# Kernel tuning notes

Hardware: AMD Instinct MI355X
Metric: run time of the kernel (lower is better)

Reference implementation:

```python
import jax, jax.numpy as jnp
import numpy as np

B, N, D = 16, 4096, 256
EPS = 1e-6


def setup_inputs() -> dict:
    key = jax.random.key(0)
    kq, kk, kv, kwq, kwk, kbq, kbk = jax.random.split(key, 7)
    s = 1.0 / np.sqrt(D)
    return {
        "Q": jax.random.normal(kq, (B, N, D), dtype=jnp.float32),
        "K": jax.random.normal(kk, (B, N, D), dtype=jnp.float32),
        "V": jax.random.normal(kv, (B, N, D), dtype=jnp.float32),
        "Wq": jax.random.normal(kwq, (D, D), dtype=jnp.float32) * s,
        "bq": jax.random.normal(kbq, (D,), dtype=jnp.float32) * 0.01,
        "Wk": jax.random.normal(kwk, (D, D), dtype=jnp.float32) * s,
        "bk": jax.random.normal(kbk, (D,), dtype=jnp.float32) * 0.01,
    }


def reference(Q, K, V, Wq, bq, Wk, bk):
    # phi feature maps: sigmoid(Linear(dim, dim)) as in Flow-Attention
    phi_q = jax.nn.sigmoid(jnp.einsum("bnd,de->bne", Q, Wq) + bq)  # [B,N,D]
    phi_k = jax.nn.sigmoid(jnp.einsum("bnd,de->bne", K, Wk) + bk)  # [B,N,D]
    # O: column-normalized phi_k (over sequence); I: row-normalized phi_q (over features)
    O = phi_k / (jnp.sum(phi_k, axis=1, keepdims=True) + EPS)  # [B,N,D]
    I = phi_q / (jnp.sum(phi_q, axis=2, keepdims=True) + EPS)  # [B,N,D]
    # competition over the sequence dim
    V_b = jax.nn.softmax(O * V, axis=1)  # [B,N,D]
    # linear attention: (phi_k^T @ V_b) is the small [B,D,D] state
    KV = jnp.einsum("bnd,bne->bde", phi_k, V_b)  # [B,D,D]
    A = jnp.einsum("bnd,bde->bne", I, KV)  # [B,N,D]
    # sigmoid allocation gate
    R = jax.nn.sigmoid(jnp.sum(phi_q, axis=2, keepdims=True)) * A
    return R
```

## Files before the change

### kernel.cpp

```cpp
#include <hip/hip_runtime.h>
#include <cstddef>

#define EPS_ 1e-6f

typedef unsigned short u16;
typedef __attribute__((ext_vector_type(8))) short short8;
typedef __attribute__((ext_vector_type(8))) unsigned short us8;
typedef __attribute__((ext_vector_type(4))) unsigned short us4;
typedef __attribute__((ext_vector_type(4))) float f32x4;

__device__ __forceinline__ float sigmoidf_(float x){ return 1.0f/(1.0f+__expf(-x)); }
__device__ __forceinline__ u16 f2bf(float x){
  union { float f; unsigned i; } c; c.f = x;
  unsigned r = c.i + 0x7FFFu + ((c.i >> 16) & 1u);
  return (u16)(r >> 16);
}
__device__ __forceinline__ float bf2f(u16 u){
  union { unsigned i; float f; } c; c.i = ((unsigned)u) << 16; return c.f;
}

__global__ __launch_bounds__(256) void prep_w(const float* __restrict__ Wq,
                                              const float* __restrict__ Wk,
                                              u16* __restrict__ WqT,
                                              u16* __restrict__ WkT){
  const int e = blockIdx.x & 255;
  const float* W = (blockIdx.x < 256) ? Wq : Wk;
  u16* WT = (blockIdx.x < 256) ? WqT : WkT;
  const int d = threadIdx.x;
  WT[e*256 + d] = f2bf(W[d*256 + e]);
}

template<bool TRANS>
__global__ __launch_bounds__(256) void phi_gemm(const float* __restrict__ X,
    const u16* __restrict__ WT, const float* __restrict__ bias,
    u16* __restrict__ outp, float* __restrict__ sums)
{
  __shared__ u16 A_lds[128][40];
  __shared__ u16 B_lds[128][40];
  __shared__ u16 T_lds[TRANS ? 128*136 : 2];

  const int t = threadIdx.x;
  const int l = t & 63;
  const int w = t >> 6;
  const int wm = w & 1, wf = w >> 1;
  const int row0 = blockIdx.x * 128;
  const int f0   = blockIdx.y * 128;

  f32x4 acc[4][4];
  #pragma unroll
  for (int i=0;i<4;i++)
    #pragma unroll
    for (int j=0;j<4;j++) acc[i][j] = (f32x4){0.f,0.f,0.f,0.f};

  const int kq = t & 7, nsub = t >> 3;
  const int fr = t >> 2, fq = t & 3;
  const int kof = (l >> 4) * 8;

  for (int k0 = 0; k0 < 256; k0 += 32) {
    #pragma unroll
    for (int p = 0; p < 4; p++) {
      int n = p*32 + nsub;
      float4 v = *(const float4*)&X[(size_t)(row0+n)*256 + k0 + kq*4];
      us4 h; h[0]=f2bf(v.x); h[1]=f2bf(v.y); h[2]=f2bf(v.z); h[3]=f2bf(v.w);
      *(us4*)&A_lds[n][kq*4] = h;
    }
    #pragma unroll
    for (int p = 0; p < 2; p++) {
      int f = p*64 + fr;
      *(us8*)&B_lds[f][fq*8] = *(const us8*)&WT[(size_t)(f0+f)*256 + k0 + fq*8];
    }
    __syncthreads();
    short8 af[4], bfr[4];
    #pragma unroll
    for (int mi=0;mi<4;mi++) af[mi]  = *(const short8*)&A_lds[wm*64 + mi*16 + (l&15)][kof];
    #pragma unroll
    for (int fi=0;fi<4;fi++) bfr[fi] = *(const short8*)&B_lds[wf*64 + fi*16 + (l&15)][kof];
    #pragma unroll
    for (int mi=0;mi<4;mi++)
      #pragma unroll
      for (int fi=0;fi<4;fi++)
        acc[mi][fi] = __builtin_amdgcn_mfma_f32_16x16x32_bf16(af[mi], bfr[fi], acc[mi][fi], 0,0,0);
    __syncthreads();
  }

  float bfv[4];
  #pragma unroll
  for (int fi=0;fi<4;fi++) bfv[fi] = bias[f0 + wf*64 + fi*16 + (l&15)];

  if (!TRANS) {
    #pragma unroll
    for (int mi=0;mi<4;mi++) {
      float ph[4][4];
      #pragma unroll
      for (int fi=0;fi<4;fi++)
        #pragma unroll
        for (int r=0;r<4;r++)
          ph[fi][r] = sigmoidf_(acc[mi][fi][r] + bfv[fi]);
      #pragma unroll
      for (int r=0;r<4;r++){
        int row = row0 + wm*64 + mi*16 + (l>>4)*4 + r;
        #pragma unroll
        for (int fi=0;fi<4;fi++)
          outp[(size_t)row*256 + f0 + wf*64 + fi*16 + (l&15)] = f2bf(ph[fi][r]);
        float s = ph[0][r]+ph[1][r]+ph[2][r]+ph[3][r];
        s += __shfl_xor(s,1); s += __shfl_xor(s,2); s += __shfl_xor(s,4); s += __shfl_xor(s,8);
        if ((l & 15) == 0) atomicAdd(&sums[row], s);
      }
    }
  } else {
    const int b = row0 >> 12;
    float cpart[4] = {0.f,0.f,0.f,0.f};
    #pragma unroll
    for (int mi=0;mi<4;mi++) {
      #pragma unroll
      for (int fi=0;fi<4;fi++){
        #pragma unroll
        for (int r=0;r<4;r++){
          float ph = sigmoidf_(acc[mi][fi][r] + bfv[fi]);
          cpart[fi] += ph;
          int fl = wf*64 + fi*16 + (l&15);
          int nl = wm*64 + mi*16 + (l>>4)*4 + r;
          T_lds[fl*136 + nl] = f2bf(ph);
        }
      }
    }
    #pragma unroll
    for (int fi=0;fi<4;fi++){
      float s = cpart[fi];
      s += __shfl_xor(s,16); s += __shfl_xor(s,32);
      if (l < 16) atomicAdd(&sums[b*256 + f0 + wf*64 + fi*16 + l], s);
    }
    __syncthreads();
    const int frr = t >> 1, st = (t & 1)*64;
    size_t gbase = ((size_t)(b*256 + f0 + frr))*4096 + (row0 & 4095);
    #pragma unroll
    for (int j=0;j<8;j++)
      *(us8*)&outp[gbase + st + j*8] = *(const us8*)&T_lds[frr*136 + st + j*8];
  }
}

__global__ __launch_bounds__(256) void kv_kernel(const u16* __restrict__ phi_kT,
    const float* __restrict__ V, const float* __restrict__ colsum,
    float* __restrict__ parts, float* __restrict__ denom)
{
  __shared__ u16  phiT_lds[256][72];
  __shared__ float V_lds[64][68];
  __shared__ u16  E_lds[64][72];

  const int t = threadIdx.x;
  const int l = t & 63;
  const int w = t >> 6;
  const int e0    = blockIdx.x * 64;
  const int nc    = blockIdx.y;
  const int b     = blockIdx.z;
  const int nbase = nc * 512;

  const int eown = t & 63;
  const int nq   = (t >> 6) * 16;
  const float inv_cs = 1.0f / (colsum[b*256 + e0 + eown] + EPS_);
  float dsum = 0.f;

  const int drow = t >> 3, oct = t & 7;
  const int vn = t >> 4, vq = t & 15;

  f32x4 acc[4][4];
  #pragma unroll
  for (int i=0;i<4;i++)
    #pragma unroll
    for (int j=0;j<4;j++) acc[i][j] = (f32x4){0.f,0.f,0.f,0.f};

  for (int c = 0; c < 8; c++) {
    const int n0 = nbase + c*64;
    #pragma unroll
    for (int p = 0; p < 8; p++) {
      int d = p*32 + drow;
      *(us8*)&phiT_lds[d][oct*8] =
        *(const us8*)&phi_kT[((size_t)(b*256 + d))*4096 + n0 + oct*8];
    }
    #pragma unroll
    for (int p = 0; p < 4; p++) {
      int n = p*16 + vn;
      *(float4*)&V_lds[n][vq*4] =
        *(const float4*)&V[((size_t)(b*4096 + n0 + n))*256 + e0 + vq*4];
    }
    __syncthreads();
    #pragma unroll
    for (int jj = 0; jj < 2; jj++) {
      us8 pv = *(const us8*)&phiT_lds[e0 + eown][nq + jj*8];
      us8 ev;
      #pragma unroll
      for (int j = 0; j < 8; j++) {
        float ph = bf2f(pv[j]);
        float vv = V_lds[nq + jj*8 + j][eown];
        float ef = __expf(ph * inv_cs * vv);
        dsum += ef;
        ev[j] = f2bf(ef);
      }
      *(us8*)&E_lds[eown][nq + jj*8] = ev;
    }
    __syncthreads();
    #pragma unroll
    for (int kk = 0; kk < 2; kk++) {
      const int ko = kk*32 + (l>>4)*8;
      short8 af[4], bfr[4];
      #pragma unroll
      for (int mi=0;mi<4;mi++) af[mi]  = *(const short8*)&phiT_lds[w*64 + mi*16 + (l&15)][ko];
      #pragma unroll
      for (int ei=0;ei<4;ei++) bfr[ei] = *(const short8*)&E_lds[ei*16 + (l&15)][ko];
      #pragma unroll
      for (int mi=0;mi<4;mi++)
        #pragma unroll
        for (int ei=0;ei<4;ei++)
          acc[mi][ei] = __builtin_amdgcn_mfma_f32_16x16x32_bf16(af[mi], bfr[ei], acc[mi][ei],0,0,0);
    }
    __syncthreads();
  }

  atomicAdd(&denom[b*256 + e0 + eown], dsum);

  float* slice = parts + ((size_t)(nc*16 + b)) * 65536;
  #pragma unroll
  for (int mi=0;mi<4;mi++)
    #pragma unroll
    for (int ei=0;ei<4;ei++)
      #pragma unroll
      for (int r=0;r<4;r++){
        int d = w*64 + mi*16 + (l>>4)*4 + r;
        int e = e0 + ei*16 + (l&15);
        slice[(size_t)d*256 + e] = acc[mi][ei][r];
      }
}

__global__ __launch_bounds__(256) void kv_norm(const float* __restrict__ parts,
    const float* __restrict__ denom, u16* __restrict__ KV_nT)
{
  __shared__ float tile[64][65];
  const int t = threadIdx.x;
  const int d0 = blockIdx.x*64, e0 = blockIdx.y*64, b = blockIdx.z;
  const int i = t >> 4, jq = t & 15;
  #pragma unroll
  for (int p=0;p<4;p++){
    int dl = p*16 + i;
    float4 s = {0.f,0.f,0.f,0.f};
    for (int nc=0;nc<8;nc++){
      const float4 v = *(const float4*)&parts[(((size_t)(nc*16 + b))*256 + d0 + dl)*256 + e0 + jq*4];
      s.x+=v.x; s.y+=v.y; s.z+=v.z; s.w+=v.w;
    }
    tile[dl][jq*4+0]=s.x; tile[dl][jq*4+1]=s.y; tile[dl][jq*4+2]=s.z; tile[dl][jq*4+3]=s.w;
  }
  __syncthreads();
  const int el = t >> 4, dq = t & 15;
  #pragma unroll
  for (int p=0;p<4;p++){
    int e = p*16 + el;
    float dn = denom[b*256 + e0 + e];
    us4 o;
    #pragma unroll
    for (int r=0;r<4;r++) o[r] = f2bf(tile[dq*4+r][e] / dn);
    *(us4*)&KV_nT[((size_t)(b*256 + e0 + e))*256 + d0 + dq*4] = o;
  }
}

__global__ __launch_bounds__(256) void out_gemm(const u16* __restrict__ phi_q,
    const u16* __restrict__ KV_nT, const float* __restrict__ rowsum,
    float* __restrict__ outp)
{
  __shared__ u16 A_lds[128][40];
  __shared__ u16 B_lds[128][40];
  __shared__ float rs_lds[128];

  const int t = threadIdx.x;
  const int l = t & 63;
  const int w = t >> 6;
  const int wm = w & 1, we = w >> 1;
  const int n0 = blockIdx.x * 128;
  const int e0 = blockIdx.y * 128;
  const int b  = blockIdx.z;

  if (t < 128) rs_lds[t] = rowsum[b*4096 + n0 + t];

  f32x4 acc[4][4];
  #pragma unroll
  for (int i=0;i<4;i++)
    #pragma unroll
    for (int j=0;j<4;j++) acc[i][j] = (f32x4){0.f,0.f,0.f,0.f};

  const int nr4 = t >> 2, q4 = t & 3;
  const int kof = (l>>4)*8;

  for (int k0 = 0; k0 < 256; k0 += 32) {
    #pragma unroll
    for (int p=0;p<2;p++){
      int n = p*64 + nr4;
      *(us8*)&A_lds[n][q4*8] = *(const us8*)&phi_q[((size_t)(b*4096 + n0 + n))*256 + k0 + q4*8];
      *(us8*)&B_lds[n][q4*8] = *(const us8*)&KV_nT[((size_t)(b*256 + e0 + n))*256 + k0 + q4*8];
    }
    __syncthreads();
    short8 af[4], bfr[4];
    #pragma unroll
    for (int mi=0;mi<4;mi++) af[mi]  = *(const short8*)&A_lds[wm*64+mi*16+(l&15)][kof];
    #pragma unroll
    for (int ei=0;ei<4;ei++) bfr[ei] = *(const short8*)&B_lds[we*64+ei*16+(l&15)][kof];
    #pragma unroll
    for (int mi=0;mi<4;mi++)
      #pragma unroll
      for (int ei=0;ei<4;ei++)
        acc[mi][ei] = __builtin_amdgcn_mfma_f32_16x16x32_bf16(af[mi], bfr[ei], acc[mi][ei],0,0,0);
    __syncthreads();
  }

  #pragma unroll
  for (int mi=0;mi<4;mi++){
    #pragma unroll
    for (int r=0;r<4;r++){
      int nl = wm*64 + mi*16 + (l>>4)*4 + r;
      float rs = rs_lds[nl];
      float gate = sigmoidf_(rs) / (rs + EPS_);
      #pragma unroll
      for (int ei=0;ei<4;ei++)
        outp[((size_t)(b*4096 + n0 + nl))*256 + e0 + we*64 + ei*16 + (l&15)] = gate*acc[mi][ei][r];
    }
  }
}

extern "C" void kernel_launch(void* const* d_in, const int* in_sizes, int n_in,
                              void* d_out, int out_size, void* d_ws, size_t ws_size,
                              hipStream_t stream) {
  const float* Q  = (const float*)d_in[0];
  const float* K  = (const float*)d_in[1];
  const float* V  = (const float*)d_in[2];
  const float* Wq = (const float*)d_in[3];
  const float* bq = (const float*)d_in[4];
  const float* Wk = (const float*)d_in[5];
  const float* bk = (const float*)d_in[6];
  float* out = (float*)d_out;

  u16* phi_q  = (u16*)d_ws;
  u16* phi_kT = phi_q + 16777216;
  u16* WqT    = phi_kT + 16777216;
  u16* WkT    = WqT + 65536;
  float* colsum = (float*)(WkT + 65536);
  float* denom  = colsum + 4096;
  float* rowsum = denom + 4096;
  float* parts  = rowsum + 65536;
  u16* KV_nT  = (u16*)(parts + 8388608);

  hipMemsetAsync(colsum, 0, (4096 + 4096 + 65536) * sizeof(float), stream);

  prep_w<<<dim3(512), 256, 0, stream>>>(Wq, Wk, WqT, WkT);
  phi_gemm<false><<<dim3(512, 2), 256, 0, stream>>>(Q, WqT, bq, phi_q, rowsum);
  phi_gemm<true ><<<dim3(512, 2), 256, 0, stream>>>(K, WkT, bk, phi_kT, colsum);
  kv_kernel<<<dim3(4, 8, 16), 256, 0, stream>>>(phi_kT, V, colsum, parts, denom);
  kv_norm<<<dim3(4, 4, 16), 256, 0, stream>>>(parts, denom, KV_nT);
  out_gemm<<<dim3(32, 2, 16), 256, 0, stream>>>(phi_q, KV_nT, rowsum, out);
}
```

Measured before the change: 331.6 us.

## Double-buffer GEMM tiles, prefetch via registers, coalesce phi stores, bf16 KV partials

Several kernels are reworked at once. phi_gemm double-buffers the X tile in LDS with register prefetch, reads the weight fragments straight from global memory, and stages outputs through LDS so global stores are coalesced. The grid order is swapped so the two feature blocks of the same rows launch next to each other. kv_kernel is split over twice as many sequence chunks with register prefetch and stores its partials in bf16, and kv_norm sums 16 bf16 partials; out_gemm is double-buffered with prefetch. Storing partials in bf16 loses accuracy in exchange for less memory traffic.

```diff
diff --git a/kernel.cpp b/kernel.cpp
--- a/kernel.cpp
+++ b/kernel.cpp
@@ -35,16 +35,27 @@
     const u16* __restrict__ WT, const float* __restrict__ bias,
     u16* __restrict__ outp, float* __restrict__ sums)
 {
-  __shared__ u16 A_lds[128][40];
-  __shared__ u16 B_lds[128][40];
-  __shared__ u16 T_lds[TRANS ? 128*136 : 2];
+  __shared__ union ShU {
+    u16 A[2][128][40];
+    u16 S[128][72];
+    u16 T[128][70];
+  } sh;
 
   const int t = threadIdx.x;
   const int l = t & 63;
   const int w = t >> 6;
   const int wm = w & 1, wf = w >> 1;
-  const int row0 = blockIdx.x * 128;
-  const int f0   = blockIdx.y * 128;
+  const int f0   = blockIdx.x * 128;
+  const int row0 = blockIdx.y * 128;
+  const int i16 = l & 15, q = l >> 4;
+
+  const int sr = t >> 3;
+  const int sk = (t & 7) * 4;
+
+  float4 pre[4];
+  #pragma unroll
+  for (int p = 0; p < 4; p++)
+    pre[p] = *(const float4*)&X[(size_t)(row0 + sr + 32*p) * 256 + sk];
 
   f32x4 acc[4][4];
   #pragma unroll
@@ -52,161 +63,195 @@
     #pragma unroll
     for (int j=0;j<4;j++) acc[i][j] = (f32x4){0.f,0.f,0.f,0.f};
 
-  const int kq = t & 7, nsub = t >> 3;
-  const int fr = t >> 2, fq = t & 3;
-  const int kof = (l >> 4) * 8;
-
-  for (int k0 = 0; k0 < 256; k0 += 32) {
-    #pragma unroll
-    for (int p = 0; p < 4; p++) {
-      int n = p*32 + nsub;
-      float4 v = *(const float4*)&X[(size_t)(row0+n)*256 + k0 + kq*4];
-      us4 h; h[0]=f2bf(v.x); h[1]=f2bf(v.y); h[2]=f2bf(v.z); h[3]=f2bf(v.w);
-      *(us4*)&A_lds[n][kq*4] = h;
-    }
-    #pragma unroll
-    for (int p = 0; p < 2; p++) {
-      int f = p*64 + fr;
-      *(us8*)&B_lds[f][fq*8] = *(const us8*)&WT[(size_t)(f0+f)*256 + k0 + fq*8];
-    }
-    __syncthreads();
-    short8 af[4], bfr[4];
-    #pragma unroll
-    for (int mi=0;mi<4;mi++) af[mi]  = *(const short8*)&A_lds[wm*64 + mi*16 + (l&15)][kof];
-    #pragma unroll
-    for (int fi=0;fi<4;fi++) bfr[fi] = *(const short8*)&B_lds[wf*64 + fi*16 + (l&15)][kof];
+  #pragma unroll
+  for (int p = 0; p < 4; p++) {
+    us4 h; h[0]=f2bf(pre[p].x); h[1]=f2bf(pre[p].y); h[2]=f2bf(pre[p].z); h[3]=f2bf(pre[p].w);
+    *(us4*)&sh.A[0][sr + 32*p][sk] = h;
+  }
+  __syncthreads();
+
+  const u16* wbase = WT + (size_t)(f0 + wf*64 + i16) * 256 + q*8;
+
+  for (int it = 0; it < 8; it++) {
+    if (it < 7) {
+      const int k0n = (it+1) * 32;
+      #pragma unroll
+      for (int p = 0; p < 4; p++)
+        pre[p] = *(const float4*)&X[(size_t)(row0 + sr + 32*p) * 256 + k0n + sk];
+    }
+    short8 bfr[4];
+    #pragma unroll
+    for (int fi=0;fi<4;fi++)
+      bfr[fi] = *(const short8*)&wbase[fi*4096 + it*32];
+    short8 af[4];
+    #pragma unroll
+    for (int mi=0;mi<4;mi++)
+      af[mi] = *(const short8*)&sh.A[it & 1][wm*64 + mi*16 + i16][q*8];
     #pragma unroll
     for (int mi=0;mi<4;mi++)
       #pragma unroll
       for (int fi=0;fi<4;fi++)
         acc[mi][fi] = __builtin_amdgcn_mfma_f32_16x16x32_bf16(af[mi], bfr[fi], acc[mi][fi], 0,0,0);
+    if (it < 7) {
+      #pragma unroll
+      for (int p = 0; p < 4; p++) {
+        us4 h; h[0]=f2bf(pre[p].x); h[1]=f2bf(pre[p].y); h[2]=f2bf(pre[p].z); h[3]=f2bf(pre[p].w);
+        *(us4*)&sh.A[(it+1)&1][sr + 32*p][sk] = h;
+      }
+    }
     __syncthreads();
   }
 
-  float bfv[4];
-  #pragma unroll
-  for (int fi=0;fi<4;fi++) bfv[fi] = bias[f0 + wf*64 + fi*16 + (l&15)];
+  float bv[4];
+  #pragma unroll
+  for (int fi=0;fi<4;fi++) bv[fi] = bias[f0 + wf*64 + fi*16 + i16];
 
   if (!TRANS) {
     #pragma unroll
-    for (int mi=0;mi<4;mi++) {
-      float ph[4][4];
-      #pragma unroll
-      for (int fi=0;fi<4;fi++)
+    for (int h = 0; h < 2; h++) {
+      if (wf == h) {
         #pragma unroll
-        for (int r=0;r<4;r++)
-          ph[fi][r] = sigmoidf_(acc[mi][fi][r] + bfv[fi]);
-      #pragma unroll
-      for (int r=0;r<4;r++){
-        int row = row0 + wm*64 + mi*16 + (l>>4)*4 + r;
-        #pragma unroll
-        for (int fi=0;fi<4;fi++)
-          outp[(size_t)row*256 + f0 + wf*64 + fi*16 + (l&15)] = f2bf(ph[fi][r]);
-        float s = ph[0][r]+ph[1][r]+ph[2][r]+ph[3][r];
-        s += __shfl_xor(s,1); s += __shfl_xor(s,2); s += __shfl_xor(s,4); s += __shfl_xor(s,8);
-        if ((l & 15) == 0) atomicAdd(&sums[row], s);
-      }
+        for (int mi=0;mi<4;mi++) {
+          float rsub[4] = {0.f,0.f,0.f,0.f};
+          #pragma unroll
+          for (int fi=0;fi<4;fi++) {
+            #pragma unroll
+            for (int r=0;r<4;r++) {
+              float ph = sigmoidf_(acc[mi][fi][r] + bv[fi]);
+              rsub[r] += ph;
+              sh.S[wm*64 + mi*16 + q*4 + r][fi*16 + i16] = f2bf(ph);
+            }
+          }
+          #pragma unroll
+          for (int r=0;r<4;r++) {
+            float s = rsub[r];
+            s += __shfl_xor(s,1); s += __shfl_xor(s,2); s += __shfl_xor(s,4); s += __shfl_xor(s,8);
+            if (i16 == 0) atomicAdd(&sums[row0 + wm*64 + mi*16 + q*4 + r], s);
+          }
+        }
+      }
+      __syncthreads();
+      #pragma unroll
+      for (int j=0;j<4;j++) {
+        int idx = t + 256*j;
+        int rr = idx >> 3, off = (idx & 7) * 8;
+        *(us8*)&outp[(size_t)(row0 + rr)*256 + f0 + h*64 + off] = *(const us8*)&sh.S[rr][off];
+      }
+      __syncthreads();
     }
   } else {
     const int b = row0 >> 12;
-    float cpart[4] = {0.f,0.f,0.f,0.f};
-    #pragma unroll
-    for (int mi=0;mi<4;mi++) {
-      #pragma unroll
-      for (int fi=0;fi<4;fi++){
+    const int nbase = row0 & 4095;
+    #pragma unroll
+    for (int h = 0; h < 2; h++) {
+      if (wm == h) {
         #pragma unroll
-        for (int r=0;r<4;r++){
-          float ph = sigmoidf_(acc[mi][fi][r] + bfv[fi]);
-          cpart[fi] += ph;
-          int fl = wf*64 + fi*16 + (l&15);
-          int nl = wm*64 + mi*16 + (l>>4)*4 + r;
-          T_lds[fl*136 + nl] = f2bf(ph);
+        for (int fi=0; fi<4; fi++) {
+          float cp = 0.f;
+          #pragma unroll
+          for (int mi=0; mi<4; mi++) {
+            us4 hv;
+            #pragma unroll
+            for (int r=0;r<4;r++){
+              float ph = sigmoidf_(acc[mi][fi][r] + bv[fi]);
+              cp += ph; hv[r] = f2bf(ph);
+            }
+            *(us4*)&sh.T[wf*64 + fi*16 + i16][mi*16 + q*4] = hv;
+          }
+          cp += __shfl_xor(cp,16); cp += __shfl_xor(cp,32);
+          if (l < 16) atomicAdd(&sums[b*256 + f0 + wf*64 + fi*16 + i16], cp);
         }
       }
-    }
-    #pragma unroll
-    for (int fi=0;fi<4;fi++){
-      float s = cpart[fi];
-      s += __shfl_xor(s,16); s += __shfl_xor(s,32);
-      if (l < 16) atomicAdd(&sums[b*256 + f0 + wf*64 + fi*16 + l], s);
-    }
-    __syncthreads();
-    const int frr = t >> 1, st = (t & 1)*64;
-    size_t gbase = ((size_t)(b*256 + f0 + frr))*4096 + (row0 & 4095);
-    #pragma unroll
-    for (int j=0;j<8;j++)
-      *(us8*)&outp[gbase + st + j*8] = *(const us8*)&T_lds[frr*136 + st + j*8];
+      __syncthreads();
+      #pragma unroll
+      for (int j=0;j<4;j++) {
+        int idx = t + 256*j;
+        int fr = idx >> 3, ch = (idx & 7) * 8;
+        *(us8*)&outp[(size_t)(b*256 + f0 + fr)*4096 + nbase + h*64 + ch] = *(const us8*)&sh.T[fr][ch];
+      }
+      __syncthreads();
+    }
   }
 }
 
 __global__ __launch_bounds__(256) void kv_kernel(const u16* __restrict__ phi_kT,
     const float* __restrict__ V, const float* __restrict__ colsum,
-    float* __restrict__ parts, float* __restrict__ denom)
+    u16* __restrict__ parts, float* __restrict__ denom)
 {
-  __shared__ u16  phiT_lds[256][72];
-  __shared__ float V_lds[64][68];
-  __shared__ u16  E_lds[64][72];
+  __shared__ u16 phiT_lds[256][72];
+  __shared__ u16 E_lds[64][72];
 
   const int t = threadIdx.x;
   const int l = t & 63;
   const int w = t >> 6;
-  const int e0    = blockIdx.x * 64;
-  const int nc    = blockIdx.y;
-  const int b     = blockIdx.z;
-  const int nbase = nc * 512;
-
-  const int eown = t & 63;
-  const int nq   = (t >> 6) * 16;
-  const float inv_cs = 1.0f / (colsum[b*256 + e0 + eown] + EPS_);
+  const int e0 = blockIdx.x * 64;
+  const int nc = blockIdx.y;
+  const int b  = blockIdx.z;
+  const int nbase = nc * 256;
+  const int i16 = l & 15, q = l >> 4;
+
+  const int sd = t >> 3;
+  const int sn = (t & 7) * 8;
+
+  us8  rA[8];
+  float rV[16];
+  {
+    #pragma unroll
+    for (int p=0;p<8;p++)
+      rA[p] = *(const us8*)&phi_kT[(size_t)(b*256 + sd + 32*p)*4096 + nbase + sn];
+    #pragma unroll
+    for (int j=0;j<16;j++)
+      rV[j] = V[(size_t)(b*4096 + nbase + w*16 + j)*256 + e0 + l];
+  }
+
+  const float inv_cs = 1.0f / (colsum[b*256 + e0 + l] + EPS_);
   float dsum = 0.f;
 
-  const int drow = t >> 3, oct = t & 7;
-  const int vn = t >> 4, vq = t & 15;
-
   f32x4 acc[4][4];
   #pragma unroll
   for (int i=0;i<4;i++)
     #pragma unroll
     for (int j=0;j<4;j++) acc[i][j] = (f32x4){0.f,0.f,0.f,0.f};
 
-  for (int c = 0; c < 8; c++) {
-    const int n0 = nbase + c*64;
-    #pragma unroll
-    for (int p = 0; p < 8; p++) {
-      int d = p*32 + drow;
-      *(us8*)&phiT_lds[d][oct*8] =
-        *(const us8*)&phi_kT[((size_t)(b*256 + d))*4096 + n0 + oct*8];
-    }
-    #pragma unroll
-    for (int p = 0; p < 4; p++) {
-      int n = p*16 + vn;
-      *(float4*)&V_lds[n][vq*4] =
-        *(const float4*)&V[((size_t)(b*4096 + n0 + n))*256 + e0 + vq*4];
-    }
+  for (int c = 0; c < 4; c++) {
+    #pragma unroll
+    for (int p=0;p<8;p++) *(us8*)&phiT_lds[sd + 32*p][sn] = rA[p];
     __syncthreads();
-    #pragma unroll
-    for (int jj = 0; jj < 2; jj++) {
-      us8 pv = *(const us8*)&phiT_lds[e0 + eown][nq + jj*8];
-      us8 ev;
-      #pragma unroll
-      for (int j = 0; j < 8; j++) {
-        float ph = bf2f(pv[j]);
-        float vv = V_lds[nq + jj*8 + j][eown];
-        float ef = __expf(ph * inv_cs * vv);
-        dsum += ef;
-        ev[j] = f2bf(ef);
-      }
-      *(us8*)&E_lds[eown][nq + jj*8] = ev;
+    const int n0n = nbase + (c+1)*64;
+    if (c < 3) {
+      #pragma unroll
+      for (int p=0;p<8;p++)
+        rA[p] = *(const us8*)&phi_kT[(size_t)(b*256 + sd + 32*p)*4096 + n0n + sn];
+    }
+    us8 pv0 = *(const us8*)&phiT_lds[e0 + l][w*16];
+    us8 pv1 = *(const us8*)&phiT_lds[e0 + l][w*16 + 8];
+    us8 ev0, ev1;
+    #pragma unroll
+    for (int j=0;j<8;j++) {
+      float ef = __expf(bf2f(pv0[j]) * inv_cs * rV[j]);
+      dsum += ef; ev0[j] = f2bf(ef);
+    }
+    #pragma unroll
+    for (int j=0;j<8;j++) {
+      float ef = __expf(bf2f(pv1[j]) * inv_cs * rV[8+j]);
+      dsum += ef; ev1[j] = f2bf(ef);
+    }
+    *(us8*)&E_lds[l][w*16]     = ev0;
+    *(us8*)&E_lds[l][w*16 + 8] = ev1;
+    if (c < 3) {
+      #pragma unroll
+      for (int j=0;j<16;j++)
+        rV[j] = V[(size_t)(b*4096 + n0n + w*16 + j)*256 + e0 + l];
     }
     __syncthreads();
     #pragma unroll
-    for (int kk = 0; kk < 2; kk++) {
-      const int ko = kk*32 + (l>>4)*8;
+    for (int kk=0;kk<2;kk++){
+      const int ko = kk*32 + q*8;
       short8 af[4], bfr[4];
       #pragma unroll
-      for (int mi=0;mi<4;mi++) af[mi]  = *(const short8*)&phiT_lds[w*64 + mi*16 + (l&15)][ko];
-      #pragma unroll
-      for (int ei=0;ei<4;ei++) bfr[ei] = *(const short8*)&E_lds[ei*16 + (l&15)][ko];
+      for (int mi=0;mi<4;mi++) af[mi]  = *(const short8*)&phiT_lds[w*64 + mi*16 + i16][ko];
+      #pragma unroll
+      for (int ei=0;ei<4;ei++) bfr[ei] = *(const short8*)&E_lds[ei*16 + i16][ko];
       #pragma unroll
       for (int mi=0;mi<4;mi++)
         #pragma unroll
@@ -216,22 +261,19 @@
     __syncthreads();
   }
 
-  atomicAdd(&denom[b*256 + e0 + eown], dsum);
-
-  float* slice = parts + ((size_t)(nc*16 + b)) * 65536;
+  atomicAdd(&denom[b*256 + e0 + l], dsum);
+
+  u16* slice = parts + ((size_t)(nc*16 + b)) * 65536;
   #pragma unroll
   for (int mi=0;mi<4;mi++)
     #pragma unroll
     for (int ei=0;ei<4;ei++)
       #pragma unroll
-      for (int r=0;r<4;r++){
-        int d = w*64 + mi*16 + (l>>4)*4 + r;
-        int e = e0 + ei*16 + (l&15);
-        slice[(size_t)d*256 + e] = acc[mi][ei][r];
-      }
-}
-
-__global__ __launch_bounds__(256) void kv_norm(const float* __restrict__ parts,
+      for (int r=0;r<4;r++)
+        slice[(size_t)(w*64 + mi*16 + q*4 + r)*256 + e0 + ei*16 + i16] = f2bf(acc[mi][ei][r]);
+}
+
+__global__ __launch_bounds__(256) void kv_norm(const u16* __restrict__ parts,
     const float* __restrict__ denom, u16* __restrict__ KV_nT)
 {
   __shared__ float tile[64][65];
@@ -241,12 +283,12 @@
   #pragma unroll
   for (int p=0;p<4;p++){
     int dl = p*16 + i;
-    float4 s = {0.f,0.f,0.f,0.f};
-    for (int nc=0;nc<8;nc++){
-      const float4 v = *(const float4*)&parts[(((size_t)(nc*16 + b))*256 + d0 + dl)*256 + e0 + jq*4];
-      s.x+=v.x; s.y+=v.y; s.z+=v.z; s.w+=v.w;
-    }
-    tile[dl][jq*4+0]=s.x; tile[dl][jq*4+1]=s.y; tile[dl][jq*4+2]=s.z; tile[dl][jq*4+3]=s.w;
+    float s0=0.f,s1=0.f,s2=0.f,s3=0.f;
+    for (int nc=0;nc<16;nc++){
+      us4 v = *(const us4*)&parts[(((size_t)(nc*16 + b))*256 + d0 + dl)*256 + e0 + jq*4];
+      s0+=bf2f(v[0]); s1+=bf2f(v[1]); s2+=bf2f(v[2]); s3+=bf2f(v[3]);
+    }
+    tile[dl][jq*4+0]=s0; tile[dl][jq*4+1]=s1; tile[dl][jq*4+2]=s2; tile[dl][jq*4+3]=s3;
   }
   __syncthreads();
   const int el = t >> 4, dq = t & 15;
@@ -265,47 +307,67 @@
     const u16* __restrict__ KV_nT, const float* __restrict__ rowsum,
     float* __restrict__ outp)
 {
-  __shared__ u16 A_lds[128][40];
-  __shared__ u16 B_lds[128][40];
+  __shared__ u16 A_lds[2][128][40];
+  __shared__ u16 B_lds[2][128][40];
   __shared__ float rs_lds[128];
 
   const int t = threadIdx.x;
   const int l = t & 63;
   const int w = t >> 6;
   const int wm = w & 1, we = w >> 1;
-  const int n0 = blockIdx.x * 128;
-  const int e0 = blockIdx.y * 128;
+  const int e0 = blockIdx.x * 128;
+  const int n0 = blockIdx.y * 128;
   const int b  = blockIdx.z;
+  const int i16 = l & 15, q = l >> 4;
 
   if (t < 128) rs_lds[t] = rowsum[b*4096 + n0 + t];
 
+  const int nr = t >> 2, q4 = (t & 3) * 8;
+  us8 pA[2], pB[2];
+  #pragma unroll
+  for (int p=0;p<2;p++){
+    pA[p] = *(const us8*)&phi_q[(size_t)(b*4096 + n0 + p*64 + nr)*256 + q4];
+    pB[p] = *(const us8*)&KV_nT[(size_t)(b*256 + e0 + p*64 + nr)*256 + q4];
+  }
+  #pragma unroll
+  for (int p=0;p<2;p++){
+    *(us8*)&A_lds[0][p*64+nr][q4] = pA[p];
+    *(us8*)&B_lds[0][p*64+nr][q4] = pB[p];
+  }
+  __syncthreads();
+
   f32x4 acc[4][4];
   #pragma unroll
   for (int i=0;i<4;i++)
     #pragma unroll
     for (int j=0;j<4;j++) acc[i][j] = (f32x4){0.f,0.f,0.f,0.f};
 
-  const int nr4 = t >> 2, q4 = t & 3;
-  const int kof = (l>>4)*8;
-
-  for (int k0 = 0; k0 < 256; k0 += 32) {
-    #pragma unroll
-    for (int p=0;p<2;p++){
-      int n = p*64 + nr4;
-      *(us8*)&A_lds[n][q4*8] = *(const us8*)&phi_q[((size_t)(b*4096 + n0 + n))*256 + k0 + q4*8];
-      *(us8*)&B_lds[n][q4*8] = *(const us8*)&KV_nT[((size_t)(b*256 + e0 + n))*256 + k0 + q4*8];
-    }
-    __syncthreads();
+  for (int it=0; it<8; it++){
+    if (it < 7) {
+      const int k0n = (it+1)*32;
+      #pragma unroll
+      for (int p=0;p<2;p++){
+        pA[p] = *(const us8*)&phi_q[(size_t)(b*4096 + n0 + p*64 + nr)*256 + k0n + q4];
+        pB[p] = *(const us8*)&KV_nT[(size_t)(b*256 + e0 + p*64 + nr)*256 + k0n + q4];
+      }
+    }
     short8 af[4], bfr[4];
     #pragma unroll
-    for (int mi=0;mi<4;mi++) af[mi]  = *(const short8*)&A_lds[wm*64+mi*16+(l&15)][kof];
-    #pragma unroll
-    for (int ei=0;ei<4;ei++) bfr[ei] = *(const short8*)&B_lds[we*64+ei*16+(l&15)][kof];
+    for (int mi=0;mi<4;mi++) af[mi]  = *(const short8*)&A_lds[it&1][wm*64+mi*16+i16][q*8];
+    #pragma unroll
+    for (int ei=0;ei<4;ei++) bfr[ei] = *(const short8*)&B_lds[it&1][we*64+ei*16+i16][q*8];
     #pragma unroll
     for (int mi=0;mi<4;mi++)
       #pragma unroll
       for (int ei=0;ei<4;ei++)
         acc[mi][ei] = __builtin_amdgcn_mfma_f32_16x16x32_bf16(af[mi], bfr[ei], acc[mi][ei],0,0,0);
+    if (it < 7) {
+      #pragma unroll
+      for (int p=0;p<2;p++){
+        *(us8*)&A_lds[(it+1)&1][p*64+nr][q4] = pA[p];
+        *(us8*)&B_lds[(it+1)&1][p*64+nr][q4] = pB[p];
+      }
+    }
     __syncthreads();
   }
 
@@ -313,12 +375,12 @@
   for (int mi=0;mi<4;mi++){
     #pragma unroll
     for (int r=0;r<4;r++){
-      int nl = wm*64 + mi*16 + (l>>4)*4 + r;
+      int nl = wm*64 + mi*16 + q*4 + r;
       float rs = rs_lds[nl];
       float gate = sigmoidf_(rs) / (rs + EPS_);
       #pragma unroll
       for (int ei=0;ei<4;ei++)
-        outp[((size_t)(b*4096 + n0 + nl))*256 + e0 + we*64 + ei*16 + (l&15)] = gate*acc[mi][ei][r];
+        outp[((size_t)(b*4096 + n0 + nl))*256 + e0 + we*64 + ei*16 + i16] = gate*acc[mi][ei][r];
     }
   }
 }
@@ -342,15 +404,15 @@
   float* colsum = (float*)(WkT + 65536);
   float* denom  = colsum + 4096;
   float* rowsum = denom + 4096;
-  float* parts  = rowsum + 65536;
-  u16* KV_nT  = (u16*)(parts + 8388608);
+  u16* parts  = (u16*)(rowsum + 65536);
+  u16* KV_nT  = parts + 16777216;
 
   hipMemsetAsync(colsum, 0, (4096 + 4096 + 65536) * sizeof(float), stream);
 
   prep_w<<<dim3(512), 256, 0, stream>>>(Wq, Wk, WqT, WkT);
-  phi_gemm<false><<<dim3(512, 2), 256, 0, stream>>>(Q, WqT, bq, phi_q, rowsum);
-  phi_gemm<true ><<<dim3(512, 2), 256, 0, stream>>>(K, WkT, bk, phi_kT, colsum);
-  kv_kernel<<<dim3(4, 8, 16), 256, 0, stream>>>(phi_kT, V, colsum, parts, denom);
+  phi_gemm<false><<<dim3(2, 512), 256, 0, stream>>>(Q, WqT, bq, phi_q, rowsum);
+  phi_gemm<true ><<<dim3(2, 512), 256, 0, stream>>>(K, WkT, bk, phi_kT, colsum);
+  kv_kernel<<<dim3(4, 16, 16), 256, 0, stream>>>(phi_kT, V, colsum, parts, denom);
   kv_norm<<<dim3(4, 4, 16), 256, 0, stream>>>(parts, denom, KV_nT);
-  out_gemm<<<dim3(32, 2, 16), 256, 0, stream>>>(phi_q, KV_nT, rowsum, out);
-}
+  out_gemm<<<dim3(2, 32, 16), 256, 0, stream>>>(phi_q, KV_nT, rowsum, out);
+}
```

Result: slower. 359.9 us (+8.5%).
